# Optimization experiments

Hardware: AMD Instinct MI355X
Metric: run time of the kernel (lower is better)

Reference implementation:

```python
import jax, jax.numpy as jnp
import numpy as np

VOCAB = 14
INPUT_SIZE = 256
HIDDEN_SIZE = 512
BATCH = 256
SEQ_LEN = 512


def setup_inputs() -> dict:
    key = jax.random.key(0)
    ks = jax.random.split(key, 16)
    concat = INPUT_SIZE + HIDDEN_SIZE
    s_in = 1.0 / np.sqrt(concat)
    s_fc = 1.0 / np.sqrt(HIDDEN_SIZE)
    inp = {
        "x": jax.random.randint(ks[0], (BATCH, SEQ_LEN), 0, VOCAB, dtype=jnp.int64),
        "lengths": jax.random.randint(ks[1], (BATCH,), 1, SEQ_LEN + 1, dtype=jnp.int64),
        "emb": jax.random.normal(ks[2], (VOCAB, INPUT_SIZE), dtype=jnp.float32),
        "Wf": jax.random.uniform(ks[3], (concat, HIDDEN_SIZE), jnp.float32, -s_in, s_in),
        "bf": jax.random.uniform(ks[4], (HIDDEN_SIZE,), jnp.float32, -s_in, s_in),
        "Wi": jax.random.uniform(ks[5], (concat, HIDDEN_SIZE), jnp.float32, -s_in, s_in),
        "bi": jax.random.uniform(ks[6], (HIDDEN_SIZE,), jnp.float32, -s_in, s_in),
        "Wc": jax.random.uniform(ks[7], (concat, HIDDEN_SIZE), jnp.float32, -s_in, s_in),
        "bc": jax.random.uniform(ks[8], (HIDDEN_SIZE,), jnp.float32, -s_in, s_in),
        "Wo": jax.random.uniform(ks[9], (concat, HIDDEN_SIZE), jnp.float32, -s_in, s_in),
        "bo": jax.random.uniform(ks[10], (HIDDEN_SIZE,), jnp.float32, -s_in, s_in),
        "fcW": jax.random.uniform(ks[11], (HIDDEN_SIZE, 1), jnp.float32, -s_fc, s_fc),
        "fcb": jax.random.uniform(ks[12], (1,), jnp.float32, -s_fc, s_fc),
    }
    return inp


def _lstm_forward(x, lengths, emb, Wf, bf, Wi, bi, Wc, bc, Wo, bo, fcW, fcb):
    B, T = x.shape
    H = Wf.shape[1]
    xe = emb[x]  # [B, T, E]
    xe_t = jnp.transpose(xe, (1, 0, 2))  # [T, B, E] for scan over time

    def step(carry, x_t):
        c, h = carry
        g = jnp.concatenate([x_t, h], axis=1)  # [B, E+H]
        f = jax.nn.sigmoid(g @ Wf + bf)
        i = jax.nn.sigmoid(g @ Wi + bi)
        c_hat = jnp.tanh(g @ Wc + bc)
        o = jax.nn.sigmoid(g @ Wo + bo)
        c_next = f * c + i * c_hat
        h_next = o * jnp.tanh(c_next)
        return (c_next, h_next), h_next

    init = (jnp.zeros((B, H), xe.dtype), jnp.zeros((B, H), xe.dtype))
    _, hs = jax.lax.scan(step, init, xe_t)  # [T, B, H]
    # hidden_outputs list = [h0(zeros), h1, ..., hT]
    hs_all = jnp.concatenate([jnp.zeros((1, B, H), xe.dtype), hs], axis=0)  # [T+1, B, H]
    last_hidden = hs_all[lengths, jnp.arange(B)]  # [B, H]
    return jax.nn.sigmoid(last_hidden @ fcW + fcb)  # [B, 1]


def reference(x, lengths, emb, Wf, bf, Wi, bi, Wc, bc, Wo, bo, fcW, fcb):
    return _lstm_forward(x, lengths, emb, Wf, bf, Wi, bi, Wc, bc, Wo, bo, fcW, fcb)
```

## Files before the change

### kernel.cpp

```cpp
#include <hip/hip_runtime.h>


typedef __attribute__((ext_vector_type(8))) short short8;
typedef __attribute__((ext_vector_type(4))) float f32x4;

#define B_      256
#define T_      512
#define H_      512
#define GC_     2048
#define VOCAB_  14
#define NG_     8
#define GSZ_    8
#define ROWS_G  32
#define SPIN_CAP 100000

#define TBL_OFF  0
#define H0_OFF   (VOCAB_ * GC_)
#define H1_OFF   (H0_OFF + 65536)
#define FLG_OFF  (H1_OFF + 65536)
#define SEN_OFF  (FLG_OFF + 256)
#define XST_OFF  (SEN_OFF + 256)
#define PERM_OFF (XST_OFF + T_ * B_)
#define SLEN_OFF (PERM_OFF + B_)

__device__ __forceinline__ ushort f2bf(float f) {
    uint u = __float_as_uint(f);
    return (ushort)((u + 0x7fffu + ((u >> 16) & 1u)) >> 16);
}
__device__ __forceinline__ float bf2f(ushort s) {
    return __uint_as_float(((uint)s) << 16);
}

__global__ void zero_f(float* p, int n) {
    int i = blockIdx.x * blockDim.x + threadIdx.x;
    int stride = gridDim.x * blockDim.x;
    for (; i < n; i += stride) p[i] = 0.f;
}

__global__ void build_table(const float* __restrict__ emb,
                            const float* __restrict__ Wf, const float* __restrict__ Wi,
                            const float* __restrict__ Wc, const float* __restrict__ Wo,
                            const float* __restrict__ bf, const float* __restrict__ bi,
                            const float* __restrict__ bc, const float* __restrict__ bo,
                            float* __restrict__ tbl) {
    int idx = blockIdx.x * 256 + threadIdx.x;
    if (idx >= VOCAB_ * GC_) return;
    int v = idx >> 11, cc = idx & 2047, u = cc >> 2, g = cc & 3;
    const float* W = (g == 0) ? Wf : (g == 1) ? Wi : (g == 2) ? Wc : Wo;
    const float* b = (g == 0) ? bf : (g == 1) ? bi : (g == 2) ? bc : bo;
    float s = b[u];
    const float* ev = emb + v * 256;
    for (int e = 0; e < 256; ++e) s += ev[e] * W[e * H_ + u];
    tbl[idx] = s;
}

__global__ void sortlen(const int* __restrict__ lengths,
                        int* __restrict__ perm, int* __restrict__ slen) {
    __shared__ int cnt[513];
    __shared__ int off[513];
    int tid = threadIdx.x;
    if (tid < 513) cnt[tid] = 0;
    __syncthreads();
    if (tid < B_) atomicAdd(&cnt[lengths[tid]], 1);
    __syncthreads();
    if (tid <= 512) {
        int s = 0;
        for (int L = tid + 1; L <= 512; ++L) s += cnt[L];
        off[tid] = s;
    }
    __syncthreads();
    if (tid < B_) {
        int L = lengths[tid];
        int p = atomicAdd(&off[L], 1);
        perm[p] = tid;
        slen[p] = L;
    }
}

__global__ void gatherx(const int* __restrict__ x, const int* __restrict__ perm,
                        int* __restrict__ xsT) {
    int t = blockIdx.x;
    int r = threadIdx.x;
    xsT[t * B_ + r] = x[perm[r] * T_ + t];
}

__global__ __launch_bounds__(512, 1) void lstm_persist(
    const float* __restrict__ Wf, const float* __restrict__ Wi,
    const float* __restrict__ Wc, const float* __restrict__ Wo,
    const float* __restrict__ tbl, const int* __restrict__ xsT,
    const int* __restrict__ slen, ushort* __restrict__ h0,
    ushort* __restrict__ h1, int* __restrict__ flg, int* __restrict__ sen) {
    const int bid = blockIdx.x;
    const int g   = bid & 7;
    const int jb  = bid >> 3;
    const int tid = threadIdx.x;
    const int w    = tid >> 6;
    const int lane = tid & 63;
    const int grow0 = g * ROWS_G;

    __shared__ float xch[8 * 32 * 36];

    short8 bfr[2][16];
    {
        const int n = lane & 15, q = lane >> 4, gg = n & 3;
        const float* Wg = (gg == 0) ? Wf : (gg == 1) ? Wi : (gg == 2) ? Wc : Wo;
#pragma unroll
        for (int nt = 0; nt < 2; ++nt) {
            int ucol = jb * 64 + w * 8 + nt * 4 + (n >> 2);
#pragma unroll
            for (int kt = 0; kt < 16; ++kt) {
                short8 bb;
#pragma unroll
                for (int jj = 0; jj < 8; ++jj) {
                    ((ushort*)&bb)[jj] = f2bf(Wg[(256 + kt * 32 + q * 8 + jj) * H_ + ucol]);
                }
                bfr[nt][kt] = bb;
            }
        }
    }

    const int tmax = slen[grow0];
    const int u_e = lane & 7, r4 = lane >> 3;
    const int ug = jb * 64 + w * 8 + u_e;
    float c[4];
    int lenr[4];
#pragma unroll
    for (int rr = 0; rr < 4; ++rr) {
        c[rr] = 0.f;
        lenr[rr] = slen[grow0 + rr * 8 + r4];
    }
    float* xw = &xch[w * 1152];
    int* myflg = &flg[g * GSZ_];
    int* mysen = &sen[g];
    const int rA = grow0 + (lane & 15);
    const int ko = (lane >> 4) * 8;

    for (int t = 0; t < tmax; ++t) {
        const ushort* hc = (t & 1) ? h1 : h0;
        ushort* hn = (t & 1) ? h0 : h1;

        f32x4 a00 = {0.f,0.f,0.f,0.f}, a01 = {0.f,0.f,0.f,0.f};
        f32x4 a10 = {0.f,0.f,0.f,0.f}, a11 = {0.f,0.f,0.f,0.f};
#pragma unroll
        for (int kt = 0; kt < 16; ++kt) {
            short8 av0 = *(const short8*)&hc[rA * H_ + kt * 32 + ko];
            short8 av1 = *(const short8*)&hc[(rA + 16) * H_ + kt * 32 + ko];
            a00 = __builtin_amdgcn_mfma_f32_16x16x32_bf16(av0, bfr[0][kt], a00, 0, 0, 0);
            a01 = __builtin_amdgcn_mfma_f32_16x16x32_bf16(av0, bfr[1][kt], a01, 0, 0, 0);
            a10 = __builtin_amdgcn_mfma_f32_16x16x32_bf16(av1, bfr[0][kt], a10, 0, 0, 0);
            a11 = __builtin_amdgcn_mfma_f32_16x16x32_bf16(av1, bfr[1][kt], a11, 0, 0, 0);
        }

        {
            int n = lane & 15, qq = (lane >> 4) * 4;
            *(f32x4*)&xw[n * 36 + qq]             = a00;
            *(f32x4*)&xw[(16 + n) * 36 + qq]      = a01;
            *(f32x4*)&xw[n * 36 + 16 + qq]        = a10;
            *(f32x4*)&xw[(16 + n) * 36 + 16 + qq] = a11;
        }

#pragma unroll
        for (int rr = 0; rr < 4; ++rr) {
            int row = rr * 8 + r4;
            int tok = xsT[t * B_ + grow0 + row];
            f32x4 tb = *(const f32x4*)&tbl[tok * GC_ + ug * 4];
            int gl = (u_e >> 2) * 16 + (u_e & 3) * 4;
            float pf = xw[(gl + 0) * 36 + row] + tb.x;
            float pi = xw[(gl + 1) * 36 + row] + tb.y;
            float pc = xw[(gl + 2) * 36 + row] + tb.z;
            float po = xw[(gl + 3) * 36 + row] + tb.w;
            float fg = 1.f / (1.f + __expf(-pf));
            float ig = 1.f / (1.f + __expf(-pi));
            float cg = 2.f / (1.f + __expf(-2.f * pc)) - 1.f;
            float og = 1.f / (1.f + __expf(-po));
            float cn = fg * c[rr] + ig * cg;
            float hh = og * (2.f / (1.f + __expf(-2.f * cn)) - 1.f);
            if (t < lenr[rr]) {
                c[rr] = cn;
                hn[(grow0 + row) * H_ + ug] = f2bf(hh);
            }
        }

        __syncthreads();
        if (tid == 0) {
            __threadfence();
            __hip_atomic_store(&myflg[jb], t + 1, __ATOMIC_RELAXED,
                               __HIP_MEMORY_SCOPE_AGENT);
        }
        if (jb == 0) {
            if (tid < GSZ_) {
                int sp = 0;
                while (__hip_atomic_load(&myflg[tid], __ATOMIC_RELAXED,
                                         __HIP_MEMORY_SCOPE_AGENT) <= t) {
                    __builtin_amdgcn_s_sleep(1);
                    if (++sp > SPIN_CAP) break;
                }
            }
            if (tid == 0) {
                __threadfence();
                __hip_atomic_store(mysen, t + 1, __ATOMIC_RELAXED,
                                   __HIP_MEMORY_SCOPE_AGENT);
            }
        } else if (tid == 0) {
            int sp = 0;
            while (__hip_atomic_load(mysen, __ATOMIC_RELAXED,
                                     __HIP_MEMORY_SCOPE_AGENT) <= t) {
                __builtin_amdgcn_s_sleep(1);
                if (++sp > SPIN_CAP) break;
            }
        }
        __syncthreads();
        __threadfence();
    }
}

__global__ void fc_out(const ushort* __restrict__ h0, const ushort* __restrict__ h1,
                       const float* __restrict__ fcW, const float* __restrict__ fcb,
                       const int* __restrict__ perm, const int* __restrict__ slen,
                       float* __restrict__ out) {
    int r = blockIdx.x;
    int lane = threadIdx.x;
    const ushort* h = (((slen[r] & 1) ? h1 : h0)) + r * H_;
    float s = 0.f;
    for (int j = lane; j < H_; j += 64) s += bf2f(h[j]) * fcW[j];
#pragma unroll
    for (int o = 32; o > 0; o >>= 1) s += __shfl_down(s, o);
    if (lane == 0) {
        out[perm[r]] = 1.f / (1.f + expf(-(s + fcb[0])));
    }
}

extern "C" void kernel_launch(void* const* d_in, const int* in_sizes, int n_in,
                              void* d_out, int out_size, void* d_ws, size_t ws_size,
                              hipStream_t stream) {
    const int* x   = (const int*)d_in[0];
    const int* len = (const int*)d_in[1];
    const float* emb = (const float*)d_in[2];
    const float* Wf  = (const float*)d_in[3];
    const float* bfp = (const float*)d_in[4];
    const float* Wi  = (const float*)d_in[5];
    const float* bip = (const float*)d_in[6];
    const float* Wc  = (const float*)d_in[7];
    const float* bcp = (const float*)d_in[8];
    const float* Wo  = (const float*)d_in[9];
    const float* bop = (const float*)d_in[10];
    const float* fcW = (const float*)d_in[11];
    const float* fcb = (const float*)d_in[12];
    float* out = (float*)d_out;

    float* wsf = (float*)d_ws;
    float*  tbl  = wsf + TBL_OFF;
    ushort* h0   = (ushort*)(wsf + H0_OFF);
    ushort* h1   = (ushort*)(wsf + H1_OFF);
    int*    flg  = (int*)(wsf + FLG_OFF);
    int*    sen  = (int*)(wsf + SEN_OFF);
    int*    xsT  = (int*)(wsf + XST_OFF);
    int*    perm = (int*)(wsf + PERM_OFF);
    int*    slen = (int*)(wsf + SLEN_OFF);

    zero_f<<<512, 256, 0, stream>>>(wsf + H0_OFF, 2 * 65536 + 512);
    build_table<<<(VOCAB_ * GC_ + 255) / 256, 256, 0, stream>>>(
        emb, Wf, Wi, Wc, Wo, bfp, bip, bcp, bop, tbl);
    sortlen<<<1, 1024, 0, stream>>>(len, perm, slen);
    gatherx<<<T_, B_, 0, stream>>>(x, perm, xsT);

    lstm_persist<<<NG_ * GSZ_, 512, 0, stream>>>(
        Wf, Wi, Wc, Wo, tbl, xsT, slen, h0, h1, flg, sen);

    fc_out<<<B_, 64, 0, stream>>>(h0, h1, fcW, fcb, perm, slen, out);
}
```

Before: 9.219 ms.

## Replace two-level sentinel barrier with flat flag wait and coherent atomic h accesses

The per-step group barrier no longer routes through a leader block and sentinel. Every block now polls all eight peer flags directly, and the __threadfence calls are dropped. To stay correct without the fences, h reads and writes become relaxed agent-scope atomics, with neighbouring lanes packing two bf16 values into one 32-bit store. The aim is a shorter barrier chain per timestep, at the cost of more polling traffic and dword-granular loads in place of 128-bit vector loads.

```diff
diff --git a/kernel.cpp b/kernel.cpp
--- a/kernel.cpp
+++ b/kernel.cpp
@@ -89,7 +89,7 @@
     const float* __restrict__ Wc, const float* __restrict__ Wo,
     const float* __restrict__ tbl, const int* __restrict__ xsT,
     const int* __restrict__ slen, ushort* __restrict__ h0,
-    ushort* __restrict__ h1, int* __restrict__ flg, int* __restrict__ sen) {
+    ushort* __restrict__ h1, int* __restrict__ flg) {
     const int bid = blockIdx.x;
     const int g   = bid & 7;
     const int jb  = bid >> 3;
@@ -131,24 +131,33 @@
     }
     float* xw = &xch[w * 1152];
     int* myflg = &flg[g * GSZ_];
-    int* mysen = &sen[g];
     const int rA = grow0 + (lane & 15);
     const int ko = (lane >> 4) * 8;
+    const int baseA0 = (rA * H_ + ko) >> 1;
+    const int baseA1 = ((rA + 16) * H_ + ko) >> 1;
+
+    union U8 { uint u[4]; short8 s; };
 
     for (int t = 0; t < tmax; ++t) {
-        const ushort* hc = (t & 1) ? h1 : h0;
+        const uint* hcu = (const uint*)((t & 1) ? h1 : h0);
         ushort* hn = (t & 1) ? h0 : h1;
 
         f32x4 a00 = {0.f,0.f,0.f,0.f}, a01 = {0.f,0.f,0.f,0.f};
         f32x4 a10 = {0.f,0.f,0.f,0.f}, a11 = {0.f,0.f,0.f,0.f};
 #pragma unroll
         for (int kt = 0; kt < 16; ++kt) {
-            short8 av0 = *(const short8*)&hc[rA * H_ + kt * 32 + ko];
-            short8 av1 = *(const short8*)&hc[(rA + 16) * H_ + kt * 32 + ko];
-            a00 = __builtin_amdgcn_mfma_f32_16x16x32_bf16(av0, bfr[0][kt], a00, 0, 0, 0);
-            a01 = __builtin_amdgcn_mfma_f32_16x16x32_bf16(av0, bfr[1][kt], a01, 0, 0, 0);
-            a10 = __builtin_amdgcn_mfma_f32_16x16x32_bf16(av1, bfr[0][kt], a10, 0, 0, 0);
-            a11 = __builtin_amdgcn_mfma_f32_16x16x32_bf16(av1, bfr[1][kt], a11, 0, 0, 0);
+            U8 c0, c1;
+#pragma unroll
+            for (int q = 0; q < 4; ++q) {
+                c0.u[q] = __hip_atomic_load((uint*)&hcu[baseA0 + kt * 16 + q],
+                                            __ATOMIC_RELAXED, __HIP_MEMORY_SCOPE_AGENT);
+                c1.u[q] = __hip_atomic_load((uint*)&hcu[baseA1 + kt * 16 + q],
+                                            __ATOMIC_RELAXED, __HIP_MEMORY_SCOPE_AGENT);
+            }
+            a00 = __builtin_amdgcn_mfma_f32_16x16x32_bf16(c0.s, bfr[0][kt], a00, 0, 0, 0);
+            a01 = __builtin_amdgcn_mfma_f32_16x16x32_bf16(c0.s, bfr[1][kt], a01, 0, 0, 0);
+            a10 = __builtin_amdgcn_mfma_f32_16x16x32_bf16(c1.s, bfr[0][kt], a10, 0, 0, 0);
+            a11 = __builtin_amdgcn_mfma_f32_16x16x32_bf16(c1.s, bfr[1][kt], a11, 0, 0, 0);
         }
 
         {
@@ -175,42 +184,30 @@
             float og = 1.f / (1.f + __expf(-po));
             float cn = fg * c[rr] + ig * cg;
             float hh = og * (2.f / (1.f + __expf(-2.f * cn)) - 1.f);
+            float hp = __shfl_xor(hh, 1);
             if (t < lenr[rr]) {
                 c[rr] = cn;
-                hn[(grow0 + row) * H_ + ug] = f2bf(hh);
+                if (!(lane & 1)) {
+                    uint hv = (uint)f2bf(hh) | ((uint)f2bf(hp) << 16);
+                    __hip_atomic_store((uint*)&hn[(grow0 + row) * H_ + ug], hv,
+                                       __ATOMIC_RELAXED, __HIP_MEMORY_SCOPE_AGENT);
+                }
             }
         }
 
         __syncthreads();
-        if (tid == 0) {
-            __threadfence();
+        if (tid == 0)
             __hip_atomic_store(&myflg[jb], t + 1, __ATOMIC_RELAXED,
                                __HIP_MEMORY_SCOPE_AGENT);
-        }
-        if (jb == 0) {
-            if (tid < GSZ_) {
-                int sp = 0;
-                while (__hip_atomic_load(&myflg[tid], __ATOMIC_RELAXED,
-                                         __HIP_MEMORY_SCOPE_AGENT) <= t) {
-                    __builtin_amdgcn_s_sleep(1);
-                    if (++sp > SPIN_CAP) break;
-                }
-            }
-            if (tid == 0) {
-                __threadfence();
-                __hip_atomic_store(mysen, t + 1, __ATOMIC_RELAXED,
-                                   __HIP_MEMORY_SCOPE_AGENT);
-            }
-        } else if (tid == 0) {
+        if (tid < GSZ_) {
             int sp = 0;
-            while (__hip_atomic_load(mysen, __ATOMIC_RELAXED,
+            while (__hip_atomic_load(&myflg[tid], __ATOMIC_RELAXED,
                                      __HIP_MEMORY_SCOPE_AGENT) <= t) {
                 __builtin_amdgcn_s_sleep(1);
                 if (++sp > SPIN_CAP) break;
             }
         }
         __syncthreads();
-        __threadfence();
     }
 }
 
@@ -253,7 +250,6 @@
     ushort* h0   = (ushort*)(wsf + H0_OFF);
     ushort* h1   = (ushort*)(wsf + H1_OFF);
     int*    flg  = (int*)(wsf + FLG_OFF);
-    int*    sen  = (int*)(wsf + SEN_OFF);
     int*    xsT  = (int*)(wsf + XST_OFF);
     int*    perm = (int*)(wsf + PERM_OFF);
     int*    slen = (int*)(wsf + SLEN_OFF);
@@ -265,7 +261,7 @@
     gatherx<<<T_, B_, 0, stream>>>(x, perm, xsT);
 
     lstm_persist<<<NG_ * GSZ_, 512, 0, stream>>>(
-        Wf, Wi, Wc, Wo, tbl, xsT, slen, h0, h1, flg, sen);
+        Wf, Wi, Wc, Wo, tbl, xsT, slen, h0, h1, flg);
 
     fc_out<<<B_, 64, 0, stream>>>(h0, h1, fcW, fcb, perm, slen, out);
 }
```

Result: slower. 15.87 ms (+72.2%).
